# Kernel optimization log

Measured on AMD Instinct MI355X. Metric: run time of the kernel, lower is better.

The kernel has to match this reference:

```python
import jax, jax.numpy as jnp
import numpy as np

B, T, N, C_IN = 8, 16, 2048, 2
H, C_OUT = 64, 64
KT, K = 3, 3
E = 32768


def setup_inputs() -> dict:
    key = jax.random.key(0)
    ks = jax.random.split(key, 8)
    X = jax.random.normal(ks[0], (B, T, N, C_IN), jnp.float32)
    edge_index = jax.random.randint(ks[1], (2, E), 0, N, dtype=jnp.int64)
    edge_weight = jax.random.uniform(ks[2], (E,), jnp.float32)
    conv1_w = jax.random.normal(ks[3], (2 * H, C_IN, KT, 1), jnp.float32) * 0.1
    conv1_b = jnp.zeros((2 * H,), jnp.float32)
    cheb_w = jax.random.normal(ks[4], (K, H, H), jnp.float32) * 0.05
    cheb_b = jnp.zeros((H,), jnp.float32)
    conv2_w = jax.random.normal(ks[5], (2 * C_OUT, H, KT, 1), jnp.float32) * 0.05
    conv2_b = jnp.zeros((2 * C_OUT,), jnp.float32)
    return dict(X=X, edge_index=edge_index, edge_weight=edge_weight,
                conv1_w=conv1_w, conv1_b=conv1_b, cheb_w=cheb_w, cheb_b=cheb_b,
                conv2_w=conv2_w, conv2_b=conv2_b)


def temporal_conv(x, w, b, c_out, kt):
    # x: [B, T, N, C_in] -> [B, T-kt+1, N, c_out]; causal conv (valid) + GLU with aligned residual
    xc = jnp.transpose(x, (0, 3, 1, 2))  # [B, C, T, N]
    bsz, c_in, t, n = xc.shape
    if c_in < c_out:
        x_in = jnp.concatenate([xc, jnp.zeros((bsz, c_out - c_in, t, n), xc.dtype)], axis=1)
    else:
        x_in = xc  # c_in == c_out case here (Align identity)
    x_in = x_in[:, :, kt - 1:, :]
    y = jax.lax.conv_general_dilated(xc, w, (1, 1), 'VALID',
                                     dimension_numbers=('NCHW', 'OIHW', 'NCHW'))
    y = y + b[None, :, None, None]  # [B, 2*c_out, T-kt+1, N]
    x_p, x_q = y[:, :c_out], y[:, c_out:]
    out = (x_p + x_in) * jax.nn.sigmoid(x_q)  # GLU
    return jnp.transpose(out, (0, 2, 3, 1))  # [B, T', N, c_out]


def cheb_conv(x, src, dst, ew, W, bias):
    # x: [G, N, H]. PyG ChebConv, sym normalization, lambda_max=2 =>
    # L_hat = -D^{-1/2} A D^{-1/2} with zero diagonal (self-loops removed/cancelled).
    n = x.shape[1]
    w = jnp.where(src == dst, jnp.zeros_like(ew), ew)  # remove self loops
    deg = jnp.zeros((n,), x.dtype).at[src].add(w)
    deg_safe = jnp.where(deg > 0, deg, jnp.ones_like(deg))
    dis = jnp.where(deg > 0, jax.lax.rsqrt(deg_safe), jnp.zeros_like(deg))
    wn = -dis[src] * w * dis[dst]  # scaled Laplacian edge weights

    def lhat(z):  # sparse L_hat @ z, batched over graph dim
        return jnp.zeros_like(z).at[:, dst].add(z[:, src] * wn[None, :, None])

    tx0 = x
    out = jnp.einsum('gnh,ho->gno', tx0, W[0])
    tx1 = lhat(x)
    out = out + jnp.einsum('gnh,ho->gno', tx1, W[1])
    for k in range(2, W.shape[0]):
        tx2 = 2.0 * lhat(tx1) - tx0
        out = out + jnp.einsum('gnh,ho->gno', tx2, W[k])
        tx0, tx1 = tx1, tx2
    return out + bias


def reference(X, edge_index, edge_weight, conv1_w, conv1_b, cheb_w, cheb_b, conv2_w, conv2_b):
    t0 = temporal_conv(X, conv1_w, conv1_b, H, KT)      # [B, T-2, N, H]
    bsz, tm, n, h = t0.shape
    g = t0.reshape(bsz * tm, n, h)
    src, dst = edge_index[0], edge_index[1]
    tg = cheb_conv(g, src, dst, edge_weight, cheb_w, cheb_b)
    tg = jax.nn.relu(tg).reshape(bsz, tm, n, h)
    out = temporal_conv(tg, conv2_w, conv2_b, C_OUT, KT)  # [B, T-4, N, C_OUT]
    # batch_norm=False, dropout=0 (eval): the permute pairs cancel -> identity
    return out
```

## Files before the change

kernel.cpp:

```cpp
#include <hip/hip_runtime.h>
#include <cstdint>

#define B_ 8
#define T_ 16
#define N_ 2048
#define CIN_ 2
#define H_ 64
#define COUT_ 64
#define KT_ 3
#define E_ 32768
#define T1_ 14
#define T2_ 12
#define G_ (B_*T1_)
#define GS_ (G_*H_)

typedef __attribute__((ext_vector_type(8))) short bf16x8;
typedef __attribute__((ext_vector_type(4))) float f32x4;
typedef unsigned short ushort_;
typedef __attribute__((ext_vector_type(8))) unsigned short u16x8;

__device__ __forceinline__ float sigmoidf_(float x){ return 1.f/(1.f+expf(-x)); }
__device__ __forceinline__ int rfl_(int x){ return __builtin_amdgcn_readfirstlane(x); }

__device__ __forceinline__ ushort_ f2b(float x){
  union {float f; uint32_t u;} v; v.f = x;
  uint32_t r = (v.u + 0x7FFFu + ((v.u>>16)&1u)) >> 16;
  return (ushort_)r;
}
__device__ __forceinline__ float b2f(ushort_ x){
  union {uint32_t u; float f;} v; v.u = ((uint32_t)x)<<16;
  return v.f;
}

__global__ void k_zero(float* __restrict__ deg, int* __restrict__ cnt, int* __restrict__ fillc){
  int i = blockIdx.x*blockDim.x + threadIdx.x;
  if(i < N_){ deg[i] = 0.f; cnt[i] = 0; fillc[i] = 0; }
}

__global__ void k_deg_cnt(const int* __restrict__ src, const int* __restrict__ dst,
                          const float* __restrict__ ew, float* deg, int* cnt){
  int e = blockIdx.x*blockDim.x + threadIdx.x;
  if(e >= E_) return;
  int s = src[e], d = dst[e];
  float w = (s==d) ? 0.f : ew[e];
  atomicAdd(&deg[s], w);
  atomicAdd(&cnt[d], 1);
}

__global__ void k_dis(const float* __restrict__ deg, float* __restrict__ dis){
  int n = blockIdx.x*blockDim.x + threadIdx.x;
  if(n >= N_) return;
  float dg = deg[n];
  dis[n] = dg > 0.f ? rsqrtf(dg) : 0.f;
}

__global__ void k_scan(const int* __restrict__ cnt, int* __restrict__ offs){
  __shared__ int sums[256];
  int tid = threadIdx.x;
  int base = tid*8;
  int loc[8]; int s = 0;
  #pragma unroll
  for(int j=0;j<8;j++){ loc[j]=s; s += cnt[base+j]; }
  sums[tid] = s; __syncthreads();
  for(int ofs=1; ofs<256; ofs<<=1){
    int t = (tid>=ofs) ? sums[tid-ofs] : 0;
    __syncthreads();
    sums[tid] += t;
    __syncthreads();
  }
  int ebase = (tid==0) ? 0 : sums[tid-1];
  #pragma unroll
  for(int j=0;j<8;j++) offs[base+j] = ebase + loc[j];
  if(tid==255) offs[N_] = sums[255];
}

__global__ void k_fill(const int* __restrict__ src, const int* __restrict__ dst,
                       const float* __restrict__ ew, const float* __restrict__ dis,
                       const int* __restrict__ offs, int* fillc,
                       int2* __restrict__ epack){
  int e = blockIdx.x*blockDim.x + threadIdx.x;
  if(e >= E_) return;
  int s = src[e], d = dst[e];
  float w = (s==d) ? 0.f : ew[e];
  float wn = -dis[s]*w*dis[d];
  int pos = offs[d] + atomicAdd(&fillc[d], 1);
  epack[pos] = make_int2(s, __float_as_int(wn));
}

__global__ void k_prep_cheb(const float* __restrict__ cw, ushort_* __restrict__ Bp){
  int i = blockIdx.x*blockDim.x + threadIdx.x;
  if(i >= 6*4*64) return;
  int lane = i & 63; int cn = i >> 6; int c = cn >> 2; int n = cn & 3;
  #pragma unroll
  for(int j=0;j<8;j++){
    int k = c*32 + (lane>>4)*8 + j;
    int h = k & 63; int m = k >> 6;
    int col = n*16 + (lane&15);
    float v;
    if(m == 0)      v = cw[(size_t)h*64 + col] - cw[(size_t)(128+h)*64 + col];
    else if(m == 1) v = cw[(size_t)(64+h)*64 + col];
    else            v = 2.f*cw[(size_t)(128+h)*64 + col];
    Bp[(size_t)i*8 + j] = f2b(v);
  }
}
__global__ void k_prep_conv2(const float* __restrict__ w2, ushort_* __restrict__ Bp2){
  int i = blockIdx.x*blockDim.x + threadIdx.x;
  if(i >= 6*8*64) return;
  int lane = i & 63; int cn = i >> 6; int c = cn >> 3; int n = cn & 7;
  #pragma unroll
  for(int j=0;j<8;j++){
    int k = c*32 + (lane>>4)*8 + j;
    int co = n*16 + (lane&15);
    int kt = k >> 6, ci = k & 63;
    Bp2[(size_t)i*8 + j] = f2b(w2[(size_t)co*192 + ci*3 + kt]);
  }
}

__global__ void k_conv1(const float* __restrict__ X, const float* __restrict__ w1,
                        const float* __restrict__ b1, ushort_* __restrict__ t0){
  int wv = rfl_(blockIdx.x*4 + (threadIdx.x>>6));
  int lane = threadIdx.x & 63;
  int nb = wv % (N_/8); int bt = wv / (N_/8); int b = bt / T1_; int t = bt % T1_;
  int n0 = nb*8;
  const float* Xp = X + ((size_t)((b*T_ + t)*N_ + n0))*CIN_;
  float wp[6], wq[6];
  #pragma unroll
  for(int k=0;k<6;k++){
    wp[k] = w1[ lane      *6 + k];
    wq[k] = w1[(lane+H_)*6 + k];
  }
  float bp = b1[lane], bq = b1[lane+H_];
  #pragma unroll
  for(int j=0;j<8;j++){
    float yp = bp, yq = bq;
    #pragma unroll
    for(int kt=0;kt<KT_;kt++)
      #pragma unroll
      for(int ci=0;ci<CIN_;ci++){
        float x = Xp[kt*(N_*CIN_) + j*CIN_ + ci];
        yp += x * wp[ci*3+kt];
        yq += x * wq[ci*3+kt];
      }
    float xin = (lane < CIN_) ? Xp[2*(N_*CIN_) + j*CIN_ + lane] : 0.f;
    t0[(size_t)(n0+j)*GS_ + (size_t)bt*H_ + lane] = f2b((yp + xin) * sigmoidf_(yq));
  }
}

__global__ void k_spmm3(const ushort_* __restrict__ zin, ushort_* __restrict__ out,
                        const int* __restrict__ offs, const int2* __restrict__ epack){
  int lane = threadIdx.x & 63;
  int wv = threadIdx.x >> 6;
  int bid = blockIdx.x;
  int work = (bid & 7)*896 + (bid >> 3);
  int gg = work >> 9;
  int dblk = work & 511;
  int d = dblk*4 + wv;
  int e0 = offs[d], e1 = offs[d+1];
  size_t lo = (size_t)(gg*8)*H_ + lane*8;
  const ushort_* zb = zin + lo;
  float ac[8] = {};
  #pragma unroll 2
  for(int i=e0;i<e1;i++){
    int2 e = epack[i];
    float w = __int_as_float(e.y);
    u16x8 zv = *(const u16x8*)(zb + (size_t)e.x*GS_);
    #pragma unroll
    for(int j=0;j<8;j++) ac[j] += w*b2f(zv[j]);
  }
  u16x8 ov;
  #pragma unroll
  for(int j=0;j<8;j++) ov[j] = f2b(ac[j]);
  *(u16x8*)(out + (size_t)d*GS_ + lo) = ov;
}

__global__ __launch_bounds__(256) void k_cheb_mfma(
    const ushort_* __restrict__ t0, const ushort_* __restrict__ tx1,
    const ushort_* __restrict__ y2, const ushort_* __restrict__ Bp,
    const float* __restrict__ bias, ushort_* __restrict__ tg){
  __shared__ ushort_ lb[6*4*64*8];
  int tid = threadIdx.x;
  #pragma unroll
  for(int i=0;i<6;i++)
    *(u16x8*)(lb + i*2048 + tid*8) = *(const u16x8*)(Bp + i*2048 + tid*8);
  __syncthreads();
  int lane = tid & 63;
  int wv = tid >> 6;
  int g = blockIdx.x >> 4;
  int row0 = (blockIdx.x & 15)*128 + wv*32;
  int ra = row0 + (lane&15);
  bf16x8 a[2][6];
  #pragma unroll
  for(int c=0;c<6;c++){
    const ushort_* s = (c>>1)==0 ? t0 : ((c>>1)==1 ? tx1 : y2);
    int eoff = (c&1)*32 + (lane>>4)*8;
    const ushort_* sb = s + (size_t)g*H_ + eoff;
    a[0][c] = *(const bf16x8*)(sb + (size_t)ra*GS_);
    a[1][c] = *(const bf16x8*)(sb + (size_t)(ra+16)*GS_);
  }
  f32x4 acc[2][4] = {};
  #pragma unroll
  for(int c=0;c<6;c++){
    #pragma unroll
    for(int n=0;n<4;n++){
      bf16x8 bfr = *(const bf16x8*)(lb + ((c*4+n)*64 + lane)*8);
      acc[0][n] = __builtin_amdgcn_mfma_f32_16x16x32_bf16(a[0][c], bfr, acc[0][n], 0,0,0);
      acc[1][n] = __builtin_amdgcn_mfma_f32_16x16x32_bf16(a[1][c], bfr, acc[1][n], 0,0,0);
    }
  }
  #pragma unroll
  for(int rg=0; rg<2; rg++)
    #pragma unroll
    for(int n=0;n<4;n++){
      int col = n*16 + (lane&15);
      float bv = bias[col];
      #pragma unroll
      for(int r=0;r<4;r++){
        int row = row0 + rg*16 + (lane>>4)*4 + r;
        float v = fmaxf(acc[rg][n][r] + bv, 0.f);
        tg[(size_t)(g*N_+row)*H_ + col] = f2b(v);
      }
    }
}

__global__ __launch_bounds__(256) void k_conv2_mfma(
    const ushort_* __restrict__ tg, const ushort_* __restrict__ Bp2,
    const float* __restrict__ b2, float* __restrict__ out){
  __shared__ ushort_ lb[6*8*64*8];
  int tid = threadIdx.x;
  #pragma unroll
  for(int i=0;i<12;i++)
    *(u16x8*)(lb + i*2048 + tid*8) = *(const u16x8*)(Bp2 + i*2048 + tid*8);
  __syncthreads();
  int lane = tid & 63;
  int wv = tid >> 6;
  int blk = blockIdx.x;
  int bt = blk >> 4; int nblk = blk & 15;
  int b = bt / T2_, t = bt % T2_;
  int n0 = nblk*128 + wv*32;
  const ushort_* base = tg + (size_t)(b*T1_ + t)*N_*H_;
  int ra = n0 + (lane&15);
  f32x4 acc[2][8] = {};
  #pragma unroll
  for(int c=0;c<6;c++){
    const ushort_* s = base + (size_t)(c>>1)*N_*H_;
    int eoff = (c&1)*32 + (lane>>4)*8;
    bf16x8 a0 = *(const bf16x8*)(s + (size_t)ra*H_ + eoff);
    bf16x8 a1 = *(const bf16x8*)(s + (size_t)(ra+16)*H_ + eoff);
    #pragma unroll
    for(int n=0;n<8;n++){
      bf16x8 bfr = *(const bf16x8*)(lb + ((c*8+n)*64 + lane)*8);
      acc[0][n] = __builtin_amdgcn_mfma_f32_16x16x32_bf16(a0, bfr, acc[0][n], 0,0,0);
      acc[1][n] = __builtin_amdgcn_mfma_f32_16x16x32_bf16(a1, bfr, acc[1][n], 0,0,0);
    }
  }
  const ushort_* xslab = base + (size_t)2*N_*H_;
  float* ob = out + (size_t)(b*T2_ + t)*N_*H_;
  #pragma unroll
  for(int rg=0;rg<2;rg++)
    #pragma unroll
    for(int n=0;n<4;n++){
      int col = n*16 + (lane&15);
      float bp = b2[col], bq = b2[col+COUT_];
      #pragma unroll
      for(int r=0;r<4;r++){
        int row = n0 + rg*16 + (lane>>4)*4 + r;
        float xin = b2f(xslab[(size_t)row*H_ + col]);
        float p = acc[rg][n][r] + bp + xin;
        float q = acc[rg][n+4][r] + bq;
        ob[(size_t)row*H_ + col] = p * sigmoidf_(q);
      }
    }
}

extern "C" void kernel_launch(void* const* d_in, const int* in_sizes, int n_in,
                              void* d_out, int out_size, void* d_ws, size_t ws_size,
                              hipStream_t stream){
  (void)in_sizes; (void)n_in; (void)out_size; (void)ws_size;
  const float* X  = (const float*)d_in[0];
  const int*   ei = (const int*)d_in[1];
  const float* ew = (const float*)d_in[2];
  const float* w1 = (const float*)d_in[3];
  const float* b1 = (const float*)d_in[4];
  const float* cw = (const float*)d_in[5];
  const float* cb = (const float*)d_in[6];
  const float* w2 = (const float*)d_in[7];
  const float* b2 = (const float*)d_in[8];
  float* out = (float*)d_out;

  char* ws = (char*)d_ws;
  const size_t BUF = (size_t)G_*N_*H_*sizeof(ushort_);
  ushort_* t0  = (ushort_*)(ws);
  ushort_* tx1 = (ushort_*)(ws + BUF);
  ushort_* y2  = (ushort_*)(ws + 2*BUF);
  ushort_* tg  = (ushort_*)(ws + 3*BUF);
  char* sm = ws + 4*BUF;
  float* deg   = (float*)(sm);
  float* dis   = (float*)(sm + 8192);
  int*   cnt   = (int*)  (sm + 16384);
  int*   fillc = (int*)  (sm + 24576);
  int*   offs  = (int*)  (sm + 32768);
  int2*  epack = (int2*) (sm + 41216);
  ushort_* Bp  = (ushort_*)(sm + 41216 + 262144);
  ushort_* Bp2 = (ushort_*)(sm + 41216 + 262144 + 24576);

  const int* src = ei;
  const int* dst = ei + E_;

  k_zero   <<<N_/256, 256, 0, stream>>>(deg, cnt, fillc);
  k_deg_cnt<<<E_/256, 256, 0, stream>>>(src, dst, ew, deg, cnt);
  k_dis    <<<N_/256, 256, 0, stream>>>(deg, dis);
  k_scan   <<<1,      256, 0, stream>>>(cnt, offs);
  k_fill   <<<E_/256, 256, 0, stream>>>(src, dst, ew, dis, offs, fillc, epack);
  k_prep_cheb <<<6, 256, 0, stream>>>(cw, Bp);
  k_prep_conv2<<<12, 256, 0, stream>>>(w2, Bp2);

  k_conv1<<<(G_*N_/8)/4, 256, 0, stream>>>(X, w1, b1, t0);

  k_spmm3<<<14*512, 256, 0, stream>>>(t0,  tx1, offs, epack);
  k_spmm3<<<14*512, 256, 0, stream>>>(tx1, y2,  offs, epack);

  k_cheb_mfma<<<G_*16, 256, 0, stream>>>(t0, tx1, y2, Bp, cb, tg);

  k_conv2_mfma<<<(B_*T2_)*16, 256, 0, stream>>>(tg, Bp2, b2, out);
}
```

Measured before the change: 160.0 us.

## Fuse second SpMM into Chebyshev MFMA kernel and merge CSR build kernels

```diff
diff --git a/kernel.cpp b/kernel.cpp
--- a/kernel.cpp
+++ b/kernel.cpp
@@ -32,87 +32,78 @@
   return v.f;
 }
 
-__global__ void k_zero(float* __restrict__ deg, int* __restrict__ cnt, int* __restrict__ fillc){
-  int i = blockIdx.x*blockDim.x + threadIdx.x;
-  if(i < N_){ deg[i] = 0.f; cnt[i] = 0; fillc[i] = 0; }
-}
-
-__global__ void k_deg_cnt(const int* __restrict__ src, const int* __restrict__ dst,
-                          const float* __restrict__ ew, float* deg, int* cnt){
-  int e = blockIdx.x*blockDim.x + threadIdx.x;
-  if(e >= E_) return;
-  int s = src[e], d = dst[e];
-  float w = (s==d) ? 0.f : ew[e];
-  atomicAdd(&deg[s], w);
-  atomicAdd(&cnt[d], 1);
-}
-
-__global__ void k_dis(const float* __restrict__ deg, float* __restrict__ dis){
-  int n = blockIdx.x*blockDim.x + threadIdx.x;
-  if(n >= N_) return;
-  float dg = deg[n];
-  dis[n] = dg > 0.f ? rsqrtf(dg) : 0.f;
-}
-
-__global__ void k_scan(const int* __restrict__ cnt, int* __restrict__ offs){
-  __shared__ int sums[256];
+__global__ __launch_bounds__(1024) void k_csr(
+    const int* __restrict__ src, const int* __restrict__ dst,
+    const float* __restrict__ ew, int* __restrict__ offs_g,
+    int2* __restrict__ epack){
+  __shared__ float degf[N_];
+  __shared__ int   cnts[N_];
+  __shared__ int   offss[N_];
+  __shared__ int   fillc[N_];
+  __shared__ int   psum[1024];
   int tid = threadIdx.x;
-  int base = tid*8;
-  int loc[8]; int s = 0;
-  #pragma unroll
-  for(int j=0;j<8;j++){ loc[j]=s; s += cnt[base+j]; }
-  sums[tid] = s; __syncthreads();
-  for(int ofs=1; ofs<256; ofs<<=1){
-    int t = (tid>=ofs) ? sums[tid-ofs] : 0;
+  for(int i=tid;i<N_;i+=1024){ degf[i]=0.f; cnts[i]=0; fillc[i]=0; }
+  __syncthreads();
+  for(int e=tid;e<E_;e+=1024){
+    int s=src[e], d=dst[e];
+    float w = (s==d)?0.f:ew[e];
+    atomicAdd(&degf[s], w);
+    atomicAdd(&cnts[d], 1);
+  }
+  __syncthreads();
+  for(int i=tid;i<N_;i+=1024){ float dg=degf[i]; degf[i] = dg>0.f? rsqrtf(dg):0.f; }
+  int b0 = cnts[tid*2], b1 = cnts[tid*2+1];
+  psum[tid] = b0+b1;
+  __syncthreads();
+  for(int ofs=1; ofs<1024; ofs<<=1){
+    int t = (tid>=ofs)? psum[tid-ofs] : 0;
     __syncthreads();
-    sums[tid] += t;
+    psum[tid] += t;
     __syncthreads();
   }
-  int ebase = (tid==0) ? 0 : sums[tid-1];
-  #pragma unroll
-  for(int j=0;j<8;j++) offs[base+j] = ebase + loc[j];
-  if(tid==255) offs[N_] = sums[255];
-}
-
-__global__ void k_fill(const int* __restrict__ src, const int* __restrict__ dst,
-                       const float* __restrict__ ew, const float* __restrict__ dis,
-                       const int* __restrict__ offs, int* fillc,
-                       int2* __restrict__ epack){
-  int e = blockIdx.x*blockDim.x + threadIdx.x;
-  if(e >= E_) return;
-  int s = src[e], d = dst[e];
-  float w = (s==d) ? 0.f : ew[e];
-  float wn = -dis[s]*w*dis[d];
-  int pos = offs[d] + atomicAdd(&fillc[d], 1);
-  epack[pos] = make_int2(s, __float_as_int(wn));
-}
-
-__global__ void k_prep_cheb(const float* __restrict__ cw, ushort_* __restrict__ Bp){
-  int i = blockIdx.x*blockDim.x + threadIdx.x;
-  if(i >= 6*4*64) return;
-  int lane = i & 63; int cn = i >> 6; int c = cn >> 2; int n = cn & 3;
-  #pragma unroll
-  for(int j=0;j<8;j++){
-    int k = c*32 + (lane>>4)*8 + j;
-    int h = k & 63; int m = k >> 6;
-    int col = n*16 + (lane&15);
-    float v;
-    if(m == 0)      v = cw[(size_t)h*64 + col] - cw[(size_t)(128+h)*64 + col];
-    else if(m == 1) v = cw[(size_t)(64+h)*64 + col];
-    else            v = 2.f*cw[(size_t)(128+h)*64 + col];
-    Bp[(size_t)i*8 + j] = f2b(v);
-  }
-}
-__global__ void k_prep_conv2(const float* __restrict__ w2, ushort_* __restrict__ Bp2){
-  int i = blockIdx.x*blockDim.x + threadIdx.x;
-  if(i >= 6*8*64) return;
-  int lane = i & 63; int cn = i >> 6; int c = cn >> 3; int n = cn & 7;
-  #pragma unroll
-  for(int j=0;j<8;j++){
-    int k = c*32 + (lane>>4)*8 + j;
-    int co = n*16 + (lane&15);
-    int kt = k >> 6, ci = k & 63;
-    Bp2[(size_t)i*8 + j] = f2b(w2[(size_t)co*192 + ci*3 + kt]);
+  int ebase = (tid==0)?0:psum[tid-1];
+  offss[tid*2]   = ebase;
+  offss[tid*2+1] = ebase + b0;
+  offs_g[tid*2]   = ebase;
+  offs_g[tid*2+1] = ebase + b0;
+  if(tid==1023) offs_g[N_] = psum[1023];
+  __syncthreads();
+  for(int e=tid;e<E_;e+=1024){
+    int s=src[e], d=dst[e];
+    float w=(s==d)?0.f:ew[e];
+    float wn = -degf[s]*w*degf[d];
+    int pos = offss[d] + atomicAdd(&fillc[d],1);
+    epack[pos] = make_int2(s, __float_as_int(wn));
+  }
+}
+
+__global__ void k_prep(const float* __restrict__ cw, const float* __restrict__ w2,
+                       ushort_* __restrict__ Bp, ushort_* __restrict__ Bp2){
+  int bi = blockIdx.x; int tid = threadIdx.x;
+  if(bi < 6){
+    int i = bi*256 + tid;
+    int lane = i & 63; int cn = i >> 6; int c = cn >> 2; int n = cn & 3;
+    #pragma unroll
+    for(int j=0;j<8;j++){
+      int k = c*32 + (lane>>4)*8 + j;
+      int h = k & 63; int m = k >> 6;
+      int col = n*16 + (lane&15);
+      float v;
+      if(m == 0)      v = cw[(size_t)h*64 + col] - cw[(size_t)(128+h)*64 + col];
+      else if(m == 1) v = cw[(size_t)(64+h)*64 + col];
+      else            v = 2.f*cw[(size_t)(128+h)*64 + col];
+      Bp[(size_t)i*8 + j] = f2b(v);
+    }
+  } else {
+    int i = (bi-6)*256 + tid;
+    int lane = i & 63; int cn = i >> 6; int c = cn >> 3; int n = cn & 7;
+    #pragma unroll
+    for(int j=0;j<8;j++){
+      int k = c*32 + (lane>>4)*8 + j;
+      int co = n*16 + (lane&15);
+      int kt = k >> 6, ci = k & 63;
+      Bp2[(size_t)i*8 + j] = f2b(w2[(size_t)co*192 + ci*3 + kt]);
+    }
   }
 }
 
@@ -173,10 +164,11 @@
   *(u16x8*)(out + (size_t)d*GS_ + lo) = ov;
 }
 
-__global__ __launch_bounds__(256) void k_cheb_mfma(
+__global__ __launch_bounds__(256) void k_cheb_fused(
     const ushort_* __restrict__ t0, const ushort_* __restrict__ tx1,
-    const ushort_* __restrict__ y2, const ushort_* __restrict__ Bp,
-    const float* __restrict__ bias, ushort_* __restrict__ tg){
+    const ushort_* __restrict__ Bp, const float* __restrict__ bias,
+    const int* __restrict__ offs, const int2* __restrict__ epack,
+    ushort_* __restrict__ tg){
   __shared__ ushort_ lb[6*4*64*8];
   int tid = threadIdx.x;
   #pragma unroll
@@ -185,17 +177,40 @@
   __syncthreads();
   int lane = tid & 63;
   int wv = tid >> 6;
-  int g = blockIdx.x >> 4;
-  int row0 = (blockIdx.x & 15)*128 + wv*32;
+  int bid = blockIdx.x;
+  int work = (bid & 7)*224 + (bid >> 3);
+  int g = work >> 4;
+  int row0 = (work & 15)*128 + wv*32;
   int ra = row0 + (lane&15);
+  int e4 = (lane>>4)*8;
   bf16x8 a[2][6];
   #pragma unroll
-  for(int c=0;c<6;c++){
-    const ushort_* s = (c>>1)==0 ? t0 : ((c>>1)==1 ? tx1 : y2);
-    int eoff = (c&1)*32 + (lane>>4)*8;
+  for(int c=0;c<4;c++){
+    const ushort_* s = (c>>1)==0 ? t0 : tx1;
+    int eoff = (c&1)*32 + e4;
     const ushort_* sb = s + (size_t)g*H_ + eoff;
     a[0][c] = *(const bf16x8*)(sb + (size_t)ra*GS_);
     a[1][c] = *(const bf16x8*)(sb + (size_t)(ra+16)*GS_);
+  }
+  const ushort_* zb = tx1 + (size_t)g*H_;
+  #pragma unroll
+  for(int rg=0;rg<2;rg++){
+    int r = ra + rg*16;
+    int e0 = offs[r], e1 = offs[r+1];
+    float a4[8] = {}, a5[8] = {};
+    for(int i=e0;i<e1;i++){
+      int2 e = epack[i];
+      float w = __int_as_float(e.y);
+      const ushort_* zr = zb + (size_t)e.x*GS_;
+      u16x8 z4 = *(const u16x8*)(zr + e4);
+      u16x8 z5 = *(const u16x8*)(zr + 32 + e4);
+      #pragma unroll
+      for(int j=0;j<8;j++){ a4[j] += w*b2f(z4[j]); a5[j] += w*b2f(z5[j]); }
+    }
+    bf16x8 p4, p5;
+    #pragma unroll
+    for(int j=0;j<8;j++){ p4[j] = (short)f2b(a4[j]); p5[j] = (short)f2b(a5[j]); }
+    a[rg][4] = p4; a[rg][5] = p5;
   }
   f32x4 acc[2][4] = {};
   #pragma unroll
@@ -291,35 +306,24 @@
   const size_t BUF = (size_t)G_*N_*H_*sizeof(ushort_);
   ushort_* t0  = (ushort_*)(ws);
   ushort_* tx1 = (ushort_*)(ws + BUF);
-  ushort_* y2  = (ushort_*)(ws + 2*BUF);
-  ushort_* tg  = (ushort_*)(ws + 3*BUF);
-  char* sm = ws + 4*BUF;
-  float* deg   = (float*)(sm);
-  float* dis   = (float*)(sm + 8192);
-  int*   cnt   = (int*)  (sm + 16384);
-  int*   fillc = (int*)  (sm + 24576);
-  int*   offs  = (int*)  (sm + 32768);
-  int2*  epack = (int2*) (sm + 41216);
-  ushort_* Bp  = (ushort_*)(sm + 41216 + 262144);
-  ushort_* Bp2 = (ushort_*)(sm + 41216 + 262144 + 24576);
+  ushort_* tg  = (ushort_*)(ws + 2*BUF);
+  char* sm = ws + 3*BUF;
+  int*   offs  = (int*)  (sm);
+  int2*  epack = (int2*) (sm + 8448);
+  ushort_* Bp  = (ushort_*)(sm + 8448 + 262144);
+  ushort_* Bp2 = (ushort_*)(sm + 8448 + 262144 + 24576);
 
   const int* src = ei;
   const int* dst = ei + E_;
 
-  k_zero   <<<N_/256, 256, 0, stream>>>(deg, cnt, fillc);
-  k_deg_cnt<<<E_/256, 256, 0, stream>>>(src, dst, ew, deg, cnt);
-  k_dis    <<<N_/256, 256, 0, stream>>>(deg, dis);
-  k_scan   <<<1,      256, 0, stream>>>(cnt, offs);
-  k_fill   <<<E_/256, 256, 0, stream>>>(src, dst, ew, dis, offs, fillc, epack);
-  k_prep_cheb <<<6, 256, 0, stream>>>(cw, Bp);
-  k_prep_conv2<<<12, 256, 0, stream>>>(w2, Bp2);
+  k_csr <<<1, 1024, 0, stream>>>(src, dst, ew, offs, epack);
+  k_prep<<<18, 256, 0, stream>>>(cw, w2, Bp, Bp2);
 
   k_conv1<<<(G_*N_/8)/4, 256, 0, stream>>>(X, w1, b1, t0);
 
-  k_spmm3<<<14*512, 256, 0, stream>>>(t0,  tx1, offs, epack);
-  k_spmm3<<<14*512, 256, 0, stream>>>(tx1, y2,  offs, epack);
-
-  k_cheb_mfma<<<G_*16, 256, 0, stream>>>(t0, tx1, y2, Bp, cb, tg);
+  k_spmm3<<<14*512, 256, 0, stream>>>(t0, tx1, offs, epack);
+
+  k_cheb_fused<<<G_*16, 256, 0, stream>>>(t0, tx1, Bp, cb, offs, epack, tg);
 
   k_conv2_mfma<<<(B_*T2_)*16, 256, 0, stream>>>(tg, Bp2, b2, out);
 }
```

Measured after the change: 247.7 us. 1.55x slower.
